# Kernel tuning notes

Measured on AMD Instinct MI355X. Metric: run time of the kernel, lower is better.

## Reference

```python
import jax, jax.numpy as jnp
import numpy as np

NUM_HEADS = 12
MODEL_SIZE = 768
HEAD_SIZE = MODEL_SIZE // NUM_HEADS
DIM = 768


def setup_inputs() -> dict:
    key = jax.random.key(0)
    ks = jax.random.split(key, 11)
    B, S, D = 4, 2048, MODEL_SIZE
    scale = 0.02
    return {
        "query": jax.random.normal(ks[0], (B, S, D), jnp.float32),
        "key": jax.random.normal(ks[1], (B, S, D), jnp.float32),
        "value": jax.random.normal(ks[2], (B, S, D), jnp.float32),
        "wq": jax.random.normal(ks[3], (D, MODEL_SIZE), jnp.float32) * scale,
        "bq": jnp.zeros((MODEL_SIZE,), jnp.float32),
        "wk": jax.random.normal(ks[4], (D, MODEL_SIZE), jnp.float32) * scale,
        "bk": jnp.zeros((MODEL_SIZE,), jnp.float32),
        "wv": jax.random.normal(ks[5], (D, MODEL_SIZE), jnp.float32) * scale,
        "bv": jnp.zeros((MODEL_SIZE,), jnp.float32),
        "wo": jax.random.normal(ks[6], (MODEL_SIZE, DIM), jnp.float32) * scale,
        "bo": jnp.zeros((DIM,), jnp.float32),
    }


def _split_heads(x):
    # [B, S, model_size] -> [B, H, S, head_size]
    B, S, _ = x.shape
    return x.reshape(B, S, NUM_HEADS, HEAD_SIZE).transpose(0, 2, 1, 3)


def reference(query, key, value, wq, bq, wk, bk, wv, bv, wo, bo):
    q = _split_heads(query @ wq + bq)   # [B,H,S,d]
    k = _split_heads(key @ wk + bk)
    v = _split_heads(value @ wv + bv)
    scale = 1.0 / jnp.sqrt(jnp.float32(HEAD_SIZE))
    score = jnp.einsum('bhqd,bhkd->bhqk', q, k) * scale
    alpha = jax.nn.softmax(score, axis=-1)
    ctx = jnp.einsum('bhqk,bhkd->bhqd', alpha, v)
    B, H, S, d = ctx.shape
    ctx = ctx.transpose(0, 2, 1, 3).reshape(B, S, H * d)
    # Dropout(0.2) is inference-mode (identity) in the original call
    return ctx @ wo + bo
```

## Files before the change

kernel.cpp:

```cpp
#include <hip/hip_runtime.h>
#include <stdint.h>

#define DEV static __device__ __forceinline__

typedef unsigned short u16;
typedef __attribute__((ext_vector_type(8))) short s16x8;
typedef __attribute__((ext_vector_type(4))) float f32x4;

DEV u16 f2bf(float x) {
    uint32_t u = __float_as_uint(x);
    u = u + 0x7FFFu + ((u >> 16) & 1u);
    return (u16)(u >> 16);
}
DEV u16 f2bf_trunc(float x) {
    return (u16)(__float_as_uint(x) >> 16);
}

DEV f32x4 mfma_bf16(s16x8 a, s16x8 b, f32x4 c) {
    return __builtin_amdgcn_mfma_f32_16x16x32_bf16(a, b, c, 0, 0, 0);
}

DEV int swz8(int bid, int nwg) { return (bid & 7) * (nwg >> 3) + (bid >> 3); }

constexpr int Bq   = 4;
constexpr int S    = 2048;
constexpr int D    = 768;
constexpr int H    = 12;
constexpr int HD   = 64;
constexpr int BS   = Bq * S;
constexpr float SC_LOG2 = 0.18033688011112042f;

DEV int4 pack8(float4 a, float4 b) {
    int4 r;
    r.x = (int)((uint32_t)f2bf(a.x) | ((uint32_t)f2bf(a.y) << 16));
    r.y = (int)((uint32_t)f2bf(a.z) | ((uint32_t)f2bf(a.w) << 16));
    r.z = (int)((uint32_t)f2bf(b.x) | ((uint32_t)f2bf(b.y) << 16));
    r.w = (int)((uint32_t)f2bf(b.z) | ((uint32_t)f2bf(b.w) << 16));
    return r;
}

__global__ __launch_bounds__(256) void k_wtrans(const float* __restrict__ w0, const float* __restrict__ w1,
                                                const float* __restrict__ w2, const float* __restrict__ w3,
                                                u16* __restrict__ t0, u16* __restrict__ t1,
                                                u16* __restrict__ t2, u16* __restrict__ t3) {
    const float* w = (blockIdx.z == 0) ? w0 : (blockIdx.z == 1) ? w1 : (blockIdx.z == 2) ? w2 : w3;
    u16*         t = (blockIdx.z == 0) ? t0 : (blockIdx.z == 1) ? t1 : (blockIdx.z == 2) ? t2 : t3;
    __shared__ float tile[64 * 65];
    const int k0 = blockIdx.y * 64, n0 = blockIdx.x * 64;
    const int tx = threadIdx.x & 15, ty = threadIdx.x >> 4;
#pragma unroll
    for (int rr = 0; rr < 4; rr++) {
        int kl = rr * 16 + ty;
        float4 v = *(const float4*)&w[(size_t)(k0 + kl) * D + n0 + tx * 4];
        tile[kl * 65 + tx * 4 + 0] = v.x;
        tile[kl * 65 + tx * 4 + 1] = v.y;
        tile[kl * 65 + tx * 4 + 2] = v.z;
        tile[kl * 65 + tx * 4 + 3] = v.w;
    }
    __syncthreads();
#pragma unroll
    for (int rr = 0; rr < 4; rr++) {
        int nl = rr * 16 + ty;
        int kl = tx * 4;
        ushort4 o = make_ushort4(f2bf(tile[(kl + 0) * 65 + nl]), f2bf(tile[(kl + 1) * 65 + nl]),
                                 f2bf(tile[(kl + 2) * 65 + nl]), f2bf(tile[(kl + 3) * 65 + nl]));
        *(ushort4*)&t[(size_t)(n0 + nl) * D + k0 + kl] = o;
    }
}

struct GemmArgs { const void* A; const u16* BT; const float* bias; void* dst; };
struct GemmArgs3 { GemmArgs g[3]; };

template <int MODE, bool AF32>
__global__ __launch_bounds__(256, 3) void k_gemm(GemmArgs3 args) {
    const int f = swz8((int)blockIdx.x, (int)gridDim.x);
    const int gy = f / 384;
    const int r = f - gy * 384;
    const int mtile = r / 6, ntile = r % 6;
    const GemmArgs& G = args.g[gy];
    const u16* __restrict__ BT = G.BT;
    const float* __restrict__ bias = G.bias;

    __shared__ __align__(16) char smem[36864];
    u16* As = (u16*)smem;
    u16* Bs = (u16*)(smem + 128 * 72 * 2);
    const int tid = threadIdx.x;
    const int lane = tid & 63;
    const int w = tid >> 6, wm = w >> 1, wn = w & 1;
    const int l16 = lane & 15, lg = lane >> 4;
    const int m0 = mtile * 128, n0 = ntile * 128;

    const int sr = tid >> 3, sp = tid & 7;

    f32x4 acc[4][4];
#pragma unroll
    for (int i = 0; i < 4; i++)
#pragma unroll
        for (int j = 0; j < 4; j++) acc[i][j] = f32x4{0.f, 0.f, 0.f, 0.f};

    int4 ar[4], br[4];
    auto load = [&](int k0) {
#pragma unroll
        for (int i = 0; i < 4; i++) {
            if (AF32) {
                const float* Af = (const float*)G.A;
                float4 x = *(const float4*)&Af[(size_t)(m0 + sr + i * 32) * D + k0 + sp * 8];
                float4 y = *(const float4*)&Af[(size_t)(m0 + sr + i * 32) * D + k0 + sp * 8 + 4];
                ar[i] = pack8(x, y);
            } else {
                ar[i] = *(const int4*)&((const u16*)G.A)[(size_t)(m0 + sr + i * 32) * D + k0 + sp * 8];
            }
            br[i] = *(const int4*)&BT[(size_t)(n0 + sr + i * 32) * D + k0 + sp * 8];
        }
    };
    load(0);
    for (int t = 0; t < 12; t++) {
        __syncthreads();
#pragma unroll
        for (int i = 0; i < 4; i++) {
            *(int4*)&As[(sr + i * 32) * 72 + sp * 8] = ar[i];
            *(int4*)&Bs[(sr + i * 32) * 72 + sp * 8] = br[i];
        }
        __syncthreads();
        if (t < 11) load((t + 1) * 64);
#pragma unroll
        for (int kk = 0; kk < 2; kk++) {
            s16x8 af[4], bf[4];
#pragma unroll
            for (int mf = 0; mf < 4; mf++)
                af[mf] = *(const s16x8*)&As[(wm * 64 + mf * 16 + l16) * 72 + kk * 32 + lg * 8];
#pragma unroll
            for (int nf = 0; nf < 4; nf++)
                bf[nf] = *(const s16x8*)&Bs[(wn * 64 + nf * 16 + l16) * 72 + kk * 32 + lg * 8];
#pragma unroll
            for (int mf = 0; mf < 4; mf++)
#pragma unroll
                for (int nf = 0; nf < 4; nf++) acc[mf][nf] = mfma_bf16(af[mf], bf[nf], acc[mf][nf]);
        }
    }
    __syncthreads();
    if (MODE == 0 && gy == 2) {
        u16* Ct = (u16*)smem;
#pragma unroll
        for (int nf = 0; nf < 4; nf++) {
            int col = wn * 64 + nf * 16 + l16;
            float bv = bias[n0 + col];
#pragma unroll
            for (int mf = 0; mf < 4; mf++) {
                int row = wm * 64 + mf * 16 + lg * 4;
#pragma unroll
                for (int rp = 0; rp < 2; rp++) {
                    uint32_t pk = (uint32_t)f2bf(acc[mf][nf][rp * 2] + bv) |
                                  ((uint32_t)f2bf(acc[mf][nf][rp * 2 + 1] + bv) << 16);
                    *(uint32_t*)&Ct[col * 136 + row + rp * 2] = pk;
                }
            }
        }
        __syncthreads();
        const int b = m0 >> 11, s0 = m0 & 2047;
#pragma unroll
        for (int i = 0; i < 8; i++) {
            int idx = i * 256 + tid;
            int col = idx >> 4, ch = idx & 15;
            int gcol = n0 + col;
            int h = gcol >> 6, dd = gcol & 63;
            int4 v = *(const int4*)&Ct[col * 136 + ch * 8];
            *(int4*)&((u16*)G.dst)[((size_t)(b * H + h) * HD + dd) * S + s0 + ch * 8] = v;
        }
    } else if (MODE == 0) {
        u16* Cs = (u16*)smem;
#pragma unroll
        for (int nf = 0; nf < 4; nf++) {
            float bv = bias[n0 + wn * 64 + nf * 16 + l16];
#pragma unroll
            for (int mf = 0; mf < 4; mf++)
#pragma unroll
                for (int rg = 0; rg < 4; rg++)
                    Cs[(wm * 64 + mf * 16 + lg * 4 + rg) * 136 + wn * 64 + nf * 16 + l16] =
                        f2bf(acc[mf][nf][rg] + bv);
        }
        __syncthreads();
#pragma unroll
        for (int i = 0; i < 8; i++) {
            int idx = i * 256 + tid;
            int row = idx >> 4, ch = idx & 15;
            int gm = m0 + row;
            int b = gm >> 11, s = gm & 2047;
            int c = ch * 8;
            int h = (n0 + c) >> 6, dd = c & 63;
            int4 v = *(const int4*)&Cs[row * 136 + c];
            *(int4*)&((u16*)G.dst)[(size_t)((b * H + h) * S + s) * HD + dd] = v;
        }
    } else {
        float* Cf = (float*)smem;
#pragma unroll
        for (int p = 0; p < 2; p++) {
            if (wm == p) {
#pragma unroll
                for (int nf = 0; nf < 4; nf++) {
                    float bv = bias[n0 + wn * 64 + nf * 16 + l16];
#pragma unroll
                    for (int mf = 0; mf < 4; mf++)
#pragma unroll
                        for (int rg = 0; rg < 4; rg++)
                            Cf[(mf * 16 + lg * 4 + rg) * 132 + wn * 64 + nf * 16 + l16] =
                                acc[mf][nf][rg] + bv;
                }
            }
            __syncthreads();
#pragma unroll
            for (int i = 0; i < 8; i++) {
                int idx = i * 256 + tid;
                int row = idx >> 5, ch = idx & 31;
                float4 v = *(const float4*)&Cf[row * 132 + ch * 4];
                *(float4*)&((float*)G.dst)[(size_t)(m0 + p * 64 + row) * D + n0 + ch * 4] = v;
            }
            if (p == 0) __syncthreads();
        }
    }
}

__global__ __launch_bounds__(512, 2) void k_attn(const u16* __restrict__ Qh,
                                                 const u16* __restrict__ Kh,
                                                 const u16* __restrict__ VT,
                                                 u16* __restrict__ CTX) {
    __shared__ u16 Ks[64 * 72];
    __shared__ u16 Vs[64 * 72];
    __shared__ u16 Ps[8][32 * 72];
    const int tid = threadIdx.x, lane = tid & 63, w = tid >> 6;
    const int l16 = lane & 15, lg = lane >> 4;
    const int f = swz8((int)blockIdx.x, (int)gridDim.x);
    const int bh = f >> 3;
    const int q0 = (f & 7) * 256 + w * 32;
    const u16* Qb = Qh + (size_t)bh * S * HD;
    const u16* Kb = Kh + (size_t)bh * S * HD;
    const u16* Vb = VT + (size_t)bh * HD * S;
    u16* Pw = &Ps[w][0];

    s16x8 qf[2][2];
#pragma unroll
    for (int mf = 0; mf < 2; mf++)
#pragma unroll
        for (int kk = 0; kk < 2; kk++)
            qf[mf][kk] = *(const s16x8*)&Qb[(size_t)(q0 + mf * 16 + l16) * HD + kk * 32 + lg * 8];

    f32x4 o[2][5];
#pragma unroll
    for (int mf = 0; mf < 2; mf++)
#pragma unroll
        for (int nf = 0; nf < 5; nf++) o[mf][nf] = f32x4{0.f, 0.f, 0.f, 0.f};

    const s16x8 ones = {0x3F80, 0x3F80, 0x3F80, 0x3F80, 0x3F80, 0x3F80, 0x3F80, 0x3F80};

    const int sr = tid >> 3, sp = tid & 7;
    int4 krg, vrg;
    auto loadkv = [&](int kv0) {
        krg = *(const int4*)&Kb[(size_t)(kv0 + sr) * HD + sp * 8];
        vrg = *(const int4*)&Vb[(size_t)sr * S + kv0 + sp * 8];
    };
    loadkv(0);
    for (int t = 0; t < S / 64; t++) {
        __syncthreads();
        *(int4*)&Ks[sr * 72 + sp * 8] = krg;
        *(int4*)&Vs[sr * 72 + sp * 8] = vrg;
        __syncthreads();
        if (t < S / 64 - 1) loadkv((t + 1) * 64);

        f32x4 sc[2][4];
#pragma unroll
        for (int mf = 0; mf < 2; mf++)
#pragma unroll
            for (int nf = 0; nf < 4; nf++) sc[mf][nf] = f32x4{0.f, 0.f, 0.f, 0.f};
#pragma unroll
        for (int kk = 0; kk < 2; kk++) {
#pragma unroll
            for (int nf = 0; nf < 4; nf++) {
                s16x8 kf = *(const s16x8*)&Ks[(nf * 16 + l16) * 72 + kk * 32 + lg * 8];
                sc[0][nf] = mfma_bf16(qf[0][kk], kf, sc[0][nf]);
                sc[1][nf] = mfma_bf16(qf[1][kk], kf, sc[1][nf]);
            }
        }
#pragma unroll
        for (int mf = 0; mf < 2; mf++)
#pragma unroll
            for (int nf = 0; nf < 4; nf++)
#pragma unroll
                for (int rg = 0; rg < 4; rg++) {
                    float p = __builtin_amdgcn_exp2f(sc[mf][nf][rg] * SC_LOG2);
                    Pw[(mf * 16 + lg * 4 + rg) * 72 + nf * 16 + l16] = f2bf_trunc(p);
                }
#pragma unroll
        for (int kk = 0; kk < 2; kk++) {
            s16x8 pf[2];
#pragma unroll
            for (int mf = 0; mf < 2; mf++)
                pf[mf] = *(const s16x8*)&Pw[(mf * 16 + l16) * 72 + kk * 32 + lg * 8];
#pragma unroll
            for (int nf = 0; nf < 4; nf++) {
                s16x8 vf = *(const s16x8*)&Vs[(nf * 16 + l16) * 72 + kk * 32 + lg * 8];
                o[0][nf] = mfma_bf16(pf[0], vf, o[0][nf]);
                o[1][nf] = mfma_bf16(pf[1], vf, o[1][nf]);
            }
            o[0][4] = mfma_bf16(pf[0], ones, o[0][4]);
            o[1][4] = mfma_bf16(pf[1], ones, o[1][4]);
        }
    }
    const int b = bh / H, h = bh - b * H;
#pragma unroll
    for (int mf = 0; mf < 2; mf++)
#pragma unroll
        for (int rg = 0; rg < 4; rg++) {
            int gq = q0 + mf * 16 + lg * 4 + rg;
            float inv = 1.0f / o[mf][4][rg];
#pragma unroll
            for (int nf = 0; nf < 4; nf++) {
                int dc = nf * 16 + l16;
                CTX[(size_t)(b * S + gq) * D + h * HD + dc] = f2bf(o[mf][nf][rg] * inv);
            }
        }
}

extern "C" void kernel_launch(void* const* d_in, const int* in_sizes, int n_in,
                              void* d_out, int out_size, void* d_ws, size_t ws_size,
                              hipStream_t stream) {
    const float* query = (const float*)d_in[0];
    const float* key   = (const float*)d_in[1];
    const float* value = (const float*)d_in[2];
    const float* wq    = (const float*)d_in[3];
    const float* bq    = (const float*)d_in[4];
    const float* wk    = (const float*)d_in[5];
    const float* bk    = (const float*)d_in[6];
    const float* wv    = (const float*)d_in[7];
    const float* bv    = (const float*)d_in[8];
    const float* wo    = (const float*)d_in[9];
    const float* bo    = (const float*)d_in[10];

    char* ws = (char*)d_ws;
    constexpr size_t SZ_ACT = (size_t)BS * D * 2;
    constexpr size_t SZ_W   = (size_t)D * D * 2;
    u16* wqT = (u16*)(ws);
    u16* wkT = (u16*)(ws + 1 * SZ_W);
    u16* wvT = (u16*)(ws + 2 * SZ_W);
    u16* woT = (u16*)(ws + 3 * SZ_W);
    char* base2 = ws + 4 * SZ_W;
    u16* Qhp = (u16*)(base2);
    u16* Khp = (u16*)(base2 + SZ_ACT);
    u16* VTp = (u16*)(base2 + 2 * SZ_ACT);
    u16* CTX = (u16*)(base2 + 3 * SZ_ACT);

    (void)in_sizes; (void)n_in; (void)out_size; (void)ws_size;

    k_wtrans<<<dim3(D / 64, D / 64, 4), 256, 0, stream>>>(wq, wk, wv, wo, wqT, wkT, wvT, woT);

    GemmArgs3 qkv;
    qkv.g[0] = {query, wqT, bq, Qhp};
    qkv.g[1] = {key,   wkT, bk, Khp};
    qkv.g[2] = {value, wvT, bv, VTp};
    k_gemm<0, true><<<dim3(3 * (BS / 128) * (D / 128)), 256, 0, stream>>>(qkv);

    k_attn<<<dim3((S / 256) * Bq * H), 512, 0, stream>>>(Qhp, Khp, VTp, CTX);

    GemmArgs3 outa;
    outa.g[0] = {CTX, woT, bo, d_out};
    outa.g[1] = outa.g[0];
    outa.g[2] = outa.g[0];
    k_gemm<1, false><<<dim3((BS / 128) * (D / 128)), 256, 0, stream>>>(outa);
}
```

Before: 388.7 us.

## Fuse all stages into one persistent cooperative kernel with grid syncs

Replaces the four kernel launches (weight transpose, QKV GEMM, attention, output GEMM) with a single cooperative persistent kernel of 512 blocks of 512 threads. Each block is split into two 256-thread halves that process GEMM tiles, and stages are separated by grid-wide syncs. Work is mapped with XCD-aware indexing. This removes launch gaps and tail effects between stages. In exchange, every stage is forced into one fixed launch shape, the block uses 72KB of shared memory, and the kernel must hit 4 blocks/CU for the cooperative launch to succeed; otherwise it falls back to separate kernels.

```diff
diff --git a/kernel.cpp b/kernel.cpp
--- a/kernel.cpp
+++ b/kernel.cpp
@@ -1,5 +1,8 @@
 #include <hip/hip_runtime.h>
+#include <hip/hip_cooperative_groups.h>
 #include <stdint.h>
+
+namespace cg = cooperative_groups;
 
 #define DEV static __device__ __forceinline__
 
@@ -39,15 +42,22 @@
     return r;
 }
 
-__global__ __launch_bounds__(256) void k_wtrans(const float* __restrict__ w0, const float* __restrict__ w1,
-                                                const float* __restrict__ w2, const float* __restrict__ w3,
-                                                u16* __restrict__ t0, u16* __restrict__ t1,
-                                                u16* __restrict__ t2, u16* __restrict__ t3) {
-    const float* w = (blockIdx.z == 0) ? w0 : (blockIdx.z == 1) ? w1 : (blockIdx.z == 2) ? w2 : w3;
-    u16*         t = (blockIdx.z == 0) ? t0 : (blockIdx.z == 1) ? t1 : (blockIdx.z == 2) ? t2 : t3;
-    __shared__ float tile[64 * 65];
-    const int k0 = blockIdx.y * 64, n0 = blockIdx.x * 64;
-    const int tx = threadIdx.x & 15, ty = threadIdx.x >> 4;
+struct MegaArgs {
+    const float *q, *k, *v;
+    const float *wq, *bq, *wk, *bk, *wv, *bv, *wo, *bo;
+    u16 *wqT, *wkT, *wvT, *woT;
+    u16 *Qhp, *Khp, *VTp, *CTX;
+    float* dout;
+};
+
+DEV void dev_wtrans(int utid, int unit, const MegaArgs& a, char* hs) {
+    const int z = unit / 144, rem = unit - z * 144;
+    const int ky = rem / 12, nx = rem % 12;
+    const float* w = (z == 0) ? a.wq : (z == 1) ? a.wk : (z == 2) ? a.wv : a.wo;
+    u16*         t = (z == 0) ? a.wqT : (z == 1) ? a.wkT : (z == 2) ? a.wvT : a.woT;
+    float* tile = (float*)hs;
+    const int k0 = ky * 64, n0 = nx * 64;
+    const int tx = utid & 15, ty = utid >> 4;
 #pragma unroll
     for (int rr = 0; rr < 4; rr++) {
         int kl = rr * 16 + ty;
@@ -68,29 +78,17 @@
     }
 }
 
-struct GemmArgs { const void* A; const u16* BT; const float* bias; void* dst; };
-struct GemmArgs3 { GemmArgs g[3]; };
-
 template <int MODE, bool AF32>
-__global__ __launch_bounds__(256, 3) void k_gemm(GemmArgs3 args) {
-    const int f = swz8((int)blockIdx.x, (int)gridDim.x);
-    const int gy = f / 384;
-    const int r = f - gy * 384;
-    const int mtile = r / 6, ntile = r % 6;
-    const GemmArgs& G = args.g[gy];
-    const u16* __restrict__ BT = G.BT;
-    const float* __restrict__ bias = G.bias;
-
-    __shared__ __align__(16) char smem[36864];
-    u16* As = (u16*)smem;
-    u16* Bs = (u16*)(smem + 128 * 72 * 2);
-    const int tid = threadIdx.x;
-    const int lane = tid & 63;
-    const int w = tid >> 6, wm = w >> 1, wn = w & 1;
+DEV void dev_gemm(int utid, int mtile, int ntile, int vt,
+                  const void* Ap, const u16* __restrict__ BT,
+                  const float* __restrict__ bias, void* dst, char* hs) {
+    u16* As = (u16*)hs;
+    u16* Bs = (u16*)(hs + 128 * 72 * 2);
+    const int lane = utid & 63;
+    const int w = utid >> 6, wm = w >> 1, wn = w & 1;
     const int l16 = lane & 15, lg = lane >> 4;
     const int m0 = mtile * 128, n0 = ntile * 128;
-
-    const int sr = tid >> 3, sp = tid & 7;
+    const int sr = utid >> 3, sp = utid & 7;
 
     f32x4 acc[4][4];
 #pragma unroll
@@ -103,12 +101,12 @@
 #pragma unroll
         for (int i = 0; i < 4; i++) {
             if (AF32) {
-                const float* Af = (const float*)G.A;
+                const float* Af = (const float*)Ap;
                 float4 x = *(const float4*)&Af[(size_t)(m0 + sr + i * 32) * D + k0 + sp * 8];
                 float4 y = *(const float4*)&Af[(size_t)(m0 + sr + i * 32) * D + k0 + sp * 8 + 4];
                 ar[i] = pack8(x, y);
             } else {
-                ar[i] = *(const int4*)&((const u16*)G.A)[(size_t)(m0 + sr + i * 32) * D + k0 + sp * 8];
+                ar[i] = *(const int4*)&((const u16*)Ap)[(size_t)(m0 + sr + i * 32) * D + k0 + sp * 8];
             }
             br[i] = *(const int4*)&BT[(size_t)(n0 + sr + i * 32) * D + k0 + sp * 8];
         }
@@ -139,8 +137,8 @@
         }
     }
     __syncthreads();
-    if (MODE == 0 && gy == 2) {
-        u16* Ct = (u16*)smem;
+    if (MODE == 0 && vt) {
+        u16* Ct = (u16*)hs;
 #pragma unroll
         for (int nf = 0; nf < 4; nf++) {
             int col = wn * 64 + nf * 16 + l16;
@@ -160,15 +158,15 @@
         const int b = m0 >> 11, s0 = m0 & 2047;
 #pragma unroll
         for (int i = 0; i < 8; i++) {
-            int idx = i * 256 + tid;
+            int idx = i * 256 + utid;
             int col = idx >> 4, ch = idx & 15;
             int gcol = n0 + col;
             int h = gcol >> 6, dd = gcol & 63;
-            int4 v = *(const int4*)&Ct[col * 136 + ch * 8];
-            *(int4*)&((u16*)G.dst)[((size_t)(b * H + h) * HD + dd) * S + s0 + ch * 8] = v;
+            int4 vv = *(const int4*)&Ct[col * 136 + ch * 8];
+            *(int4*)&((u16*)dst)[((size_t)(b * H + h) * HD + dd) * S + s0 + ch * 8] = vv;
         }
     } else if (MODE == 0) {
-        u16* Cs = (u16*)smem;
+        u16* Cs = (u16*)hs;
 #pragma unroll
         for (int nf = 0; nf < 4; nf++) {
             float bv = bias[n0 + wn * 64 + nf * 16 + l16];
@@ -182,17 +180,17 @@
         __syncthreads();
 #pragma unroll
         for (int i = 0; i < 8; i++) {
-            int idx = i * 256 + tid;
+            int idx = i * 256 + utid;
             int row = idx >> 4, ch = idx & 15;
             int gm = m0 + row;
             int b = gm >> 11, s = gm & 2047;
             int c = ch * 8;
             int h = (n0 + c) >> 6, dd = c & 63;
-            int4 v = *(const int4*)&Cs[row * 136 + c];
-            *(int4*)&((u16*)G.dst)[(size_t)((b * H + h) * S + s) * HD + dd] = v;
+            int4 vv = *(const int4*)&Cs[row * 136 + c];
+            *(int4*)&((u16*)dst)[(size_t)((b * H + h) * S + s) * HD + dd] = vv;
         }
     } else {
-        float* Cf = (float*)smem;
+        float* Cf = (float*)hs;
 #pragma unroll
         for (int p = 0; p < 2; p++) {
             if (wm == p) {
@@ -210,32 +208,28 @@
             __syncthreads();
 #pragma unroll
             for (int i = 0; i < 8; i++) {
-                int idx = i * 256 + tid;
+                int idx = i * 256 + utid;
                 int row = idx >> 5, ch = idx & 31;
-                float4 v = *(const float4*)&Cf[row * 132 + ch * 4];
-                *(float4*)&((float*)G.dst)[(size_t)(m0 + p * 64 + row) * D + n0 + ch * 4] = v;
+                float4 vv = *(const float4*)&Cf[row * 132 + ch * 4];
+                *(float4*)&((float*)dst)[(size_t)(m0 + p * 64 + row) * D + n0 + ch * 4] = vv;
             }
             if (p == 0) __syncthreads();
         }
     }
 }
 
-__global__ __launch_bounds__(512, 2) void k_attn(const u16* __restrict__ Qh,
-                                                 const u16* __restrict__ Kh,
-                                                 const u16* __restrict__ VT,
-                                                 u16* __restrict__ CTX) {
-    __shared__ u16 Ks[64 * 72];
-    __shared__ u16 Vs[64 * 72];
-    __shared__ u16 Ps[8][32 * 72];
-    const int tid = threadIdx.x, lane = tid & 63, w = tid >> 6;
+DEV void dev_attn(int tid, int f, const u16* __restrict__ Qh, const u16* __restrict__ Kh,
+                  const u16* __restrict__ VT, u16* __restrict__ CTX, char* smem) {
+    u16* Ks = (u16*)smem;
+    u16* Vs = (u16*)(smem + 9216);
+    const int lane = tid & 63, w = tid >> 6;
+    u16* Pw = (u16*)(smem + 18432 + w * 4608);
     const int l16 = lane & 15, lg = lane >> 4;
-    const int f = swz8((int)blockIdx.x, (int)gridDim.x);
     const int bh = f >> 3;
     const int q0 = (f & 7) * 256 + w * 32;
     const u16* Qb = Qh + (size_t)bh * S * HD;
     const u16* Kb = Kh + (size_t)bh * S * HD;
     const u16* Vb = VT + (size_t)bh * HD * S;
-    u16* Pw = &Ps[w][0];
 
     s16x8 qf[2][2];
 #pragma unroll
@@ -320,49 +314,106 @@
         }
 }
 
+DEV void resolve_qkv(const MegaArgs& a, int gy, const void*& A, const u16*& BT,
+                     const float*& bias, void*& dst, int& vt) {
+    if (gy == 0)      { A = a.q; BT = a.wqT; bias = a.bq; dst = a.Qhp; vt = 0; }
+    else if (gy == 1) { A = a.k; BT = a.wkT; bias = a.bk; dst = a.Khp; vt = 0; }
+    else              { A = a.v; BT = a.wvT; bias = a.bv; dst = a.VTp; vt = 1; }
+}
+
+DEV void run_qkv_tile(int utid, int f, const MegaArgs& a, char* hs) {
+    const int gy = f / 384, r = f - gy * 384;
+    const void* A; const u16* BT; const float* bias; void* dst; int vt;
+    resolve_qkv(a, gy, A, BT, bias, dst, vt);
+    dev_gemm<0, true>(utid, r / 6, r % 6, vt, A, BT, bias, dst, hs);
+}
+
+__global__ __launch_bounds__(512, 4) void k_mega(MegaArgs a) {
+    __shared__ __align__(16) char smem[73728];
+    cg::grid_group gg = cg::this_grid();
+    const int tid = threadIdx.x, bid = (int)blockIdx.x;
+    const int half = tid >> 8, utid = tid & 255;
+    const int hb = (bid << 1) | half;
+    char* hs = smem + half * 36864;
+
+    if (hb < 576) dev_wtrans(utid, hb, a, hs);
+    __threadfence(); gg.sync(); __threadfence();
+
+    {
+        const int xcd = (hb >> 1) & 7;
+        const int widx = ((hb >> 4) << 1) | (hb & 1);
+        run_qkv_tile(utid, xcd * 144 + widx, a, hs);
+        if (hb < 128)
+            run_qkv_tile(utid, xcd * 144 + 128 + widx, a, hs);
+    }
+    __threadfence(); gg.sync(); __threadfence();
+
+    if (bid < 384) dev_attn(tid, (bid & 7) * 48 + (bid >> 3), a.Qhp, a.Khp, a.VTp, a.CTX, smem);
+    __threadfence(); gg.sync(); __threadfence();
+
+    if (hb < 384) {
+        const int xcd = (hb >> 1) & 7;
+        const int widx = ((hb >> 4) << 1) | (hb & 1);
+        const int f = xcd * 48 + widx;
+        dev_gemm<1, false>(utid, f / 6, f % 6, 0, a.CTX, a.woT, a.bo, a.dout, hs);
+    }
+}
+
+__global__ __launch_bounds__(256, 4) void k_wtrans_w(MegaArgs a) {
+    __shared__ __align__(16) char s[36864];
+    const int unit = (int)blockIdx.z * 144 + (int)blockIdx.y * 12 + (int)blockIdx.x;
+    dev_wtrans(threadIdx.x, unit, a, s);
+}
+__global__ __launch_bounds__(256, 4) void k_gemm_qkv(MegaArgs a) {
+    __shared__ __align__(16) char s[36864];
+    run_qkv_tile(threadIdx.x, swz8((int)blockIdx.x, (int)gridDim.x), a, s);
+}
+__global__ __launch_bounds__(512, 2) void k_attn_w(MegaArgs a) {
+    __shared__ __align__(16) char s[55296];
+    dev_attn(threadIdx.x, swz8((int)blockIdx.x, (int)gridDim.x), a.Qhp, a.Khp, a.VTp, a.CTX, s);
+}
+__global__ __launch_bounds__(256, 4) void k_gemm_out(MegaArgs a) {
+    __shared__ __align__(16) char s[36864];
+    const int f = swz8((int)blockIdx.x, (int)gridDim.x);
+    dev_gemm<1, false>(threadIdx.x, f / 6, f % 6, 0, a.CTX, a.woT, a.bo, a.dout, s);
+}
+
 extern "C" void kernel_launch(void* const* d_in, const int* in_sizes, int n_in,
                               void* d_out, int out_size, void* d_ws, size_t ws_size,
                               hipStream_t stream) {
-    const float* query = (const float*)d_in[0];
-    const float* key   = (const float*)d_in[1];
-    const float* value = (const float*)d_in[2];
-    const float* wq    = (const float*)d_in[3];
-    const float* bq    = (const float*)d_in[4];
-    const float* wk    = (const float*)d_in[5];
-    const float* bk    = (const float*)d_in[6];
-    const float* wv    = (const float*)d_in[7];
-    const float* bv    = (const float*)d_in[8];
-    const float* wo    = (const float*)d_in[9];
-    const float* bo    = (const float*)d_in[10];
-
     char* ws = (char*)d_ws;
     constexpr size_t SZ_ACT = (size_t)BS * D * 2;
     constexpr size_t SZ_W   = (size_t)D * D * 2;
-    u16* wqT = (u16*)(ws);
-    u16* wkT = (u16*)(ws + 1 * SZ_W);
-    u16* wvT = (u16*)(ws + 2 * SZ_W);
-    u16* woT = (u16*)(ws + 3 * SZ_W);
+
+    MegaArgs a;
+    a.q  = (const float*)d_in[0];
+    a.k  = (const float*)d_in[1];
+    a.v  = (const float*)d_in[2];
+    a.wq = (const float*)d_in[3];  a.bq = (const float*)d_in[4];
+    a.wk = (const float*)d_in[5];  a.bk = (const float*)d_in[6];
+    a.wv = (const float*)d_in[7];  a.bv = (const float*)d_in[8];
+    a.wo = (const float*)d_in[9];  a.bo = (const float*)d_in[10];
+    a.wqT = (u16*)(ws);
+    a.wkT = (u16*)(ws + 1 * SZ_W);
+    a.wvT = (u16*)(ws + 2 * SZ_W);
+    a.woT = (u16*)(ws + 3 * SZ_W);
     char* base2 = ws + 4 * SZ_W;
-    u16* Qhp = (u16*)(base2);
-    u16* Khp = (u16*)(base2 + SZ_ACT);
-    u16* VTp = (u16*)(base2 + 2 * SZ_ACT);
-    u16* CTX = (u16*)(base2 + 3 * SZ_ACT);
+    a.Qhp = (u16*)(base2);
+    a.Khp = (u16*)(base2 + SZ_ACT);
+    a.VTp = (u16*)(base2 + 2 * SZ_ACT);
+    a.CTX = (u16*)(base2 + 3 * SZ_ACT);
+    a.dout = (float*)d_out;
 
     (void)in_sizes; (void)n_in; (void)out_size; (void)ws_size;
 
-    k_wtrans<<<dim3(D / 64, D / 64, 4), 256, 0, stream>>>(wq, wk, wv, wo, wqT, wkT, wvT, woT);
-
-    GemmArgs3 qkv;
-    qkv.g[0] = {query, wqT, bq, Qhp};
-    qkv.g[1] = {key,   wkT, bk, Khp};
-    qkv.g[2] = {value, wvT, bv, VTp};
-    k_gemm<0, true><<<dim3(3 * (BS / 128) * (D / 128)), 256, 0, stream>>>(qkv);
-
-    k_attn<<<dim3((S / 256) * Bq * H), 512, 0, stream>>>(Qhp, Khp, VTp, CTX);
-
-    GemmArgs3 outa;
-    outa.g[0] = {CTX, woT, bo, d_out};
-    outa.g[1] = outa.g[0];
-    outa.g[2] = outa.g[0];
-    k_gemm<1, false><<<dim3((BS / 128) * (D / 128)), 256, 0, stream>>>(outa);
-}
+    void* kargs[] = { (void*)&a };
+    hipError_t e = hipLaunchCooperativeKernel((const void*)k_mega, dim3(512), dim3(512),
+                                              kargs, 0, stream);
+    if (e != hipSuccess) {
+        (void)hipGetLastError();
+        k_wtrans_w<<<dim3(12, 12, 4), 256, 0, stream>>>(a);
+        k_gemm_qkv<<<dim3(3 * (BS / 128) * (D / 128)), 256, 0, stream>>>(a);
+        k_attn_w<<<dim3((S / 256) * Bq * H), 512, 0, stream>>>(a);
+        k_gemm_out<<<dim3((BS / 128) * (D / 128)), 256, 0, stream>>>(a);
+    }
+}
```

Result: slower. 1.192 ms (+206.8%).
